# Kernel tuning notes

Measured on AMD Instinct MI355X. Metric: run time of the kernel, lower is better.

The kernel has to match this reference:

```python
import jax, jax.numpy as jnp
import numpy as np

B, S, C, H = 2, 2048, 1024, 16
D = C // H  # head_size = 64


def setup_inputs() -> dict:
    key = jax.random.key(0)
    ks = jax.random.split(key, 8)
    scale = 1.0 / np.sqrt(C)
    return {
        "src": jax.random.normal(ks[0], (B, S, C), dtype=jnp.float32),
        "Wq": jax.random.normal(ks[1], (C, C), dtype=jnp.float32) * scale,
        "bq": jnp.zeros((C,), dtype=jnp.float32),
        "Wk": jax.random.normal(ks[2], (C, C), dtype=jnp.float32) * scale,
        "bk": jnp.zeros((C,), dtype=jnp.float32),
        "Wv": jax.random.normal(ks[3], (C, C), dtype=jnp.float32) * scale,
        "bv": jnp.zeros((C,), dtype=jnp.float32),
        "rel_k_table": jax.random.normal(ks[4], (2 * S - 1, D), dtype=jnp.float32),
    }


def reference(src, Wq, bq, Wk, bk, Wv, bv, rel_k_table):
    # Linear projections (torch Linear: x @ W.T + b)
    q = src @ Wq.T + bq  # (B,S,C)
    k = src @ Wk.T + bk
    v = src @ Wv.T + bv
    # Faithful to torch .view: raw reshape (B,S,C) -> (B,H,S,D), NOT a transpose split
    q = q.reshape(B, H, S, D)
    k = k.reshape(B, H, S, D)
    v = v.reshape(B, H, S, D)
    # content score: q @ k^T
    content = jnp.einsum("bhsd,bhtd->bhst", q, k)  # (B,H,S,S)
    # relative-position embeddings: (S,S,D)
    pos = jnp.arange(S)
    shifted = pos[None, :] - pos[:, None] + (S - 1)  # (S,S) in [0, 2S-2]
    rel_k = rel_k_table[shifted]  # (S,S,D)
    # q.view(S, B*H, D) @ rel_k.permute(0,2,1): batched over first (query-pos) axis
    q_r = q.reshape(S, B * H, D)
    pos_score = jnp.einsum("sbd,std->sbt", q_r, rel_k)  # (S,BH,S)
    pos_score = jnp.transpose(pos_score, (1, 0, 2)).reshape(B, H, S, S)
    scores = (content + pos_score) / jnp.sqrt(jnp.float32(D))
    attn = jax.nn.softmax(scores, axis=-1)
    out = jnp.einsum("bhst,bhtd->bhsd", attn, v)  # (B,H,S,D)
    out = jnp.transpose(out, (0, 2, 1, 3)).reshape(B, S, C)
    return out
```

## Files before the change

### kernel.cpp

```cpp
#include <hip/hip_runtime.h>
#include <hip/hip_bf16.h>

#define BATCH 2
#define SEQ   2048
#define CH    1024
#define NH    16
#define HD    64
#define BHN   (BATCH*NH)
#define SD    (SEQ*HD)

typedef short v8s __attribute__((ext_vector_type(8)));
typedef short v4s __attribute__((ext_vector_type(4)));
typedef float v4f __attribute__((ext_vector_type(4)));

__device__ __forceinline__ short f2bf(float f) {
    unsigned u = __float_as_uint(f);
    u += 0x7fff + ((u >> 16) & 1);
    return (short)(u >> 16);
}

__device__ __forceinline__ unsigned pk2bf(float a, float b) {
    __hip_bfloat162 h = __float22bfloat162_rn(make_float2(a, b));
    unsigned u;
    __builtin_memcpy(&u, &h, 4);
    return u;
}

__device__ __forceinline__ float ex2(float x) {
    float r; asm("v_exp_f32 %0, %1" : "=v"(r) : "v"(x)); return r;
}

#if __has_builtin(__builtin_amdgcn_perm)
#define PERMB(a, b, s) __builtin_amdgcn_perm((a), (b), (s))
#else
__device__ __forceinline__ unsigned PERMB(unsigned a, unsigned b, unsigned s) {
    unsigned r = 0;
#pragma unroll
    for (int i = 0; i < 4; i++) {
        unsigned sb = (s >> (8 * i)) & 0xff, byte;
        if (sb >= 12) byte = (sb == 12) ? 0u : 0xffu;
        else if (sb < 4) byte = (b >> (8 * sb)) & 0xff;
        else byte = (a >> (8 * (sb - 4))) & 0xff;
        r |= byte << (8 * i);
    }
    return r;
}
#endif

__device__ __forceinline__ void gl_lds16(const short* g, short* l) {
    __builtin_amdgcn_global_load_lds(
        (const __attribute__((address_space(1))) void*)g,
        (__attribute__((address_space(3))) void*)l, 16, 0, 0);
}

__global__ __launch_bounds__(256) void cast_all_kernel(
    const float* __restrict__ src, const float* __restrict__ wq,
    const float* __restrict__ wk, const float* __restrict__ wv,
    const float* __restrict__ rel,
    short* __restrict__ xb, short* __restrict__ wqb,
    short* __restrict__ wkb, short* __restrict__ wvb,
    short* __restrict__ relb)
{
    const int z = blockIdx.z;
    const float* s; short* d; int n4;
    switch (z) {
        case 0: s = src; d = xb;   n4 = 1048576; break;
        case 1: s = wq;  d = wqb;  n4 = 262144;  break;
        case 2: s = wk;  d = wkb;  n4 = 262144;  break;
        case 3: s = wv;  d = wvb;  n4 = 262144;  break;
        default: s = rel; d = relb; n4 = 65520;  break;
    }
    for (int i = blockIdx.x * 256 + threadIdx.x; i < n4; i += gridDim.x * 256) {
        float4 v = ((const float4*)s)[i];
        v4s o; o.x = f2bf(v.x); o.y = f2bf(v.y); o.z = f2bf(v.z); o.w = f2bf(v.w);
        ((v4s*)d)[i] = o;
    }
}

__global__ __launch_bounds__(256, 3) void proj_mfma_kernel(
    const short* __restrict__ Xb,
    const short* __restrict__ Wqb, const short* __restrict__ Wkb,
    const short* __restrict__ Wvb,
    const float* __restrict__ bq, const float* __restrict__ bk,
    const float* __restrict__ bv,
    short* __restrict__ qo, short* __restrict__ ko, short* __restrict__ vo)
{
    const int z = blockIdx.z;
    const short* W    = (z == 0) ? Wqb : (z == 1) ? Wkb : Wvb;
    const float* bias = (z == 0) ? bq  : (z == 1) ? bk  : bv;
    short*       out  = (z == 0) ? qo  : (z == 1) ? ko  : vo;
    const float  osc  = (z == 0) ? 0.125f * 1.44269504088896f : 1.0f;

    const int m0 = blockIdx.x * 128;
    const int n0 = blockIdx.y * 128;
    const int tid  = threadIdx.x;
    const int w    = tid >> 6;
    const int lane = tid & 63;
    const int l15  = lane & 15;
    const int quad = lane >> 4;
    const int wm = w & 1, wn = w >> 1;

    __shared__ short Al[128 * 32];
    __shared__ short Bl[128 * 32];

    v4f acc[4][4];
#pragma unroll
    for (int i = 0; i < 4; i++)
#pragma unroll
        for (int j = 0; j < 4; j++) acc[i][j] = (v4f)(0.f);

    const int lr = lane >> 2;
    const int lc = (lane & 3) * 8;

    for (int k0 = 0; k0 < 1024; k0 += 32) {
        __syncthreads();
#pragma unroll
        for (int l = 0; l < 2; l++) {
            const int slab = w * 32 + l * 16;
            gl_lds16(Xb + (size_t)(m0 + slab + lr) * 1024 + k0 + lc,
                     &Al[slab * 32]);
            gl_lds16(W + (size_t)(n0 + slab + lr) * 1024 + k0 + lc,
                     &Bl[slab * 32]);
        }
        __syncthreads();
        v8s af[4], bf[4];
#pragma unroll
        for (int mt = 0; mt < 4; mt++)
            af[mt] = *(const v8s*)&Al[(wm * 64 + mt * 16 + l15) * 32 + quad * 8];
#pragma unroll
        for (int nt = 0; nt < 4; nt++)
            bf[nt] = *(const v8s*)&Bl[(wn * 64 + nt * 16 + l15) * 32 + quad * 8];
#pragma unroll
        for (int mt = 0; mt < 4; mt++)
#pragma unroll
            for (int nt = 0; nt < 4; nt++)
                acc[mt][nt] = __builtin_amdgcn_mfma_f32_16x16x32_bf16(
                    af[mt], bf[nt], acc[mt][nt], 0, 0, 0);
    }

    float bv4[4];
#pragma unroll
    for (int nt = 0; nt < 4; nt++)
        bv4[nt] = bias[n0 + wn * 64 + nt * 16 + l15];
#pragma unroll
    for (int mt = 0; mt < 4; mt++)
#pragma unroll
        for (int rg = 0; rg < 4; rg++) {
            const int row = m0 + wm * 64 + mt * 16 + quad * 4 + rg;
#pragma unroll
            for (int nt = 0; nt < 4; nt++)
                out[(size_t)row * 1024 + n0 + wn * 64 + nt * 16 + l15] =
                    f2bf((acc[mt][nt][rg] + bv4[nt]) * osc);
        }
}

__global__ __launch_bounds__(256) void vtrans_kernel(
    const short* __restrict__ v, short* __restrict__ vt)
{
    const int bh = blockIdx.y;
    const int t0 = blockIdx.x * 64;
    const int r = threadIdx.x >> 3;
    const int c = (threadIdx.x & 7) * 8;

    __shared__ short T[64][72];
    *(v8s*)&T[r][c] =
        *(const v8s*)(v + (size_t)bh * SD + (size_t)(t0 + r) * HD + c);
    *(v8s*)&T[r + 32][c] =
        *(const v8s*)(v + (size_t)bh * SD + (size_t)(t0 + r + 32) * HD + c);
    __syncthreads();
    v8s o0, o1;
#pragma unroll
    for (int e = 0; e < 8; e++) {
        const int t = 2 * (threadIdx.x & 7) + (e >> 2) + 16 * (e & 3);
        o0[e] = T[t][r];
        o1[e] = T[t][r + 32];
    }
    *(v8s*)(vt + (size_t)bh * SD + (size_t)r * SEQ + t0 + c) = o0;
    *(v8s*)(vt + (size_t)bh * SD + (size_t)(r + 32) * SEQ + t0 + c) = o1;
}

__global__ __launch_bounds__(256, 2) void attn_mfma_kernel(
    const short* __restrict__ qb, const short* __restrict__ kb,
    const short* __restrict__ vtb, const short* __restrict__ relb,
    float* __restrict__ out)
{
    const int tid  = threadIdx.x;
    const int w    = tid >> 6;
    const int lane = tid & 63;
    const int l15  = lane & 15;
    const int quad = lane >> 4;
    const int bh = blockIdx.x, b = bh >> 4, h = bh & 15;
    const int s0 = blockIdx.y * 128;
    const int i0 = w * 32;

    __shared__ short Kl[2][64][64];
    __shared__ short Vl[2][64][64];
    __shared__ short Rl[256][64];
    __shared__ short Pb[4][2][16][64];

    v8s qc_f[2][2], qr_f[2][2];
#pragma unroll
    for (int mt = 0; mt < 2; mt++)
#pragma unroll
    for (int kh = 0; kh < 2; kh++) {
        const int row = s0 + i0 + mt * 16 + l15;
        qc_f[mt][kh] = *(const v8s*)(qb + (size_t)bh * SD +
                                     (size_t)row * HD + kh * 32 + quad * 8);
        qr_f[mt][kh] = *(const v8s*)(qb + (size_t)row * (BHN * HD) +
                                     bh * HD + kh * 32 + quad * 8);
    }

    int      slv4[4];
    unsigned selA[4], selB[4], pwoff[4];
#pragma unroll
    for (int rg = 0; rg < 4; rg++) {
        const int ii = quad * 4 + rg;
        const int e  = l15 + 15 - ii;
        const bool lo = (e < 16);
        slv4[rg] = (quad * 16 + (e & 15)) << 2;
        selA[rg] = lo ? 0x05040c0cu : 0x07060c0cu;
        selB[rg] = lo ? 0x07060c0cu : 0x01000c0cu;
        pwoff[rg] = (unsigned)(w * 4096 + ii * 128 +
                    ((((l15 >> 1) ^ (ii & 7)) << 4) + ((l15 & 1) << 3)));
    }

    const int swz = (quad ^ (l15 & 7)) << 4;
    int kaddr[2][4];
#pragma unroll
    for (int kh = 0; kh < 2; kh++) {
        const int x = kh << 6;
#pragma unroll
        for (int nt = 0; nt < 4; nt++)
            kaddr[kh][nt] = (((nt * 16 + l15) << 7) + swz) ^ x;
    }
    const int paddr0 = (l15 << 7) + swz;

    const int Bq = 1920 - s0;
    int raddr[6];
#pragma unroll
    for (int st = 0; st < 6; st++) {
        const int lg = 2032 - s0 - i0 - 16 + st * 16 + l15;
        raddr[st] = ((lg & 255) << 7) + ((quad ^ (lg & 7)) << 4);
    }

    const int strow = tid >> 3;
    const int stc   = ((tid & 7) ^ (strow & 7)) * 8;
    const short* ksrc = kb  + (size_t)bh * SD + (size_t)strow * HD  + stc;
    const short* vsrc = vtb + (size_t)bh * SD + (size_t)strow * SEQ + stc;

#pragma unroll
    for (int g = 0; g < 3; g++) {
        const int r0 = Bq + g * 64 + strow;
        const int ra = r0 < 4094 ? r0 : 4094;
        const int rb2 = (r0 + 32) < 4094 ? (r0 + 32) : 4094;
        const unsigned sl = (unsigned)((Bq + g * 64 + w * 8) & 255) << 7;
        gl_lds16(relb + (size_t)ra * HD + stc, (short*)((char*)Rl + sl));
        gl_lds16(relb + (size_t)rb2 * HD + stc, (short*)((char*)Rl + sl + 4096));
    }
    gl_lds16(ksrc,              &Kl[0][w * 8][0]);
    gl_lds16(ksrc + 32 * HD,    &Kl[0][32 + w * 8][0]);
    gl_lds16(vsrc,              &Vl[0][w * 8][0]);
    gl_lds16(vsrc + 32 * SEQ,   &Vl[0][32 + w * 8][0]);

    const short* kp = ksrc + 4096;
    const short* vp = vsrc + 64;
    const char*  relbp = (const char*)relb + stc * 2;
    unsigned roff = (unsigned)(Bq + 192 + strow) * 128;
    const unsigned ROMAX = 4094u * 128;
    unsigned rlds = (unsigned)((Bq + 192 + w * 8) & 255) << 7;

    v4f o_acc[2][4];
#pragma unroll
    for (int mt = 0; mt < 2; mt++)
#pragma unroll
        for (int nt = 0; nt < 4; nt++) o_acc[mt][nt] = (v4f)(0.f);
    float lpart[2][4] = {{0.f,0.f,0.f,0.f},{0.f,0.f,0.f,0.f}};

    v4f cacc[2][4], racc[2][5];
    unsigned g01[2][4], g23[2][4], g4v[2][4];

    auto ZACC = [&]() {
#pragma unroll
        for (int mt = 0; mt < 2; mt++) {
#pragma unroll
            for (int nt = 0; nt < 4; nt++) cacc[mt][nt] = (v4f)(0.f);
#pragma unroll
            for (int jt = 0; jt < 5; jt++) racc[mt][jt] = (v4f)(0.f);
        }
    };

    auto STAGE_K = [&](int dst) {
        short* kd = &Kl[0][w * 8][0] + (dst << 12);
        gl_lds16(kp,            kd);
        gl_lds16(kp + 32 * HD,  kd + 32 * 64);
        unsigned rc0 = roff < ROMAX ? roff : ROMAX;
        unsigned rc1 = (roff + 4096) < ROMAX ? (roff + 4096) : ROMAX;
        gl_lds16((const short*)(relbp + rc0), (short*)((char*)Rl + rlds));
        gl_lds16((const short*)(relbp + rc1), (short*)((char*)Rl + rlds + 4096));
        kp += 4096; roff += 8192; rlds = (rlds + 8192) & 32767;
    };

    auto STAGE_V = [&](int dst) {
        short* vd = &Vl[0][w * 8][0] + (dst << 12);
        gl_lds16(vp,            vd);
        gl_lds16(vp + 32 * SEQ, vd + 32 * 64);
        vp += 64;
    };

    auto QK = [&](int cur) {
        const char* kbase = (const char*)Kl + cur * 8192;
        const char* rbase = (const char*)Rl;
#pragma unroll
        for (int kh = 0; kh < 2; kh++) {
            v8s kf[4], rfj[6];
#pragma unroll
            for (int nt = 0; nt < 4; nt++)
                kf[nt] = *(const v8s*)(kbase + kaddr[kh][nt]);
#pragma unroll
            for (int st = 0; st < 6; st++)
                rfj[st] = *(const v8s*)(rbase + (raddr[st] ^ (kh << 6)));
            __builtin_amdgcn_s_setprio(1);
#pragma unroll
            for (int mt = 0; mt < 2; mt++)
#pragma unroll
                for (int nt = 0; nt < 4; nt++)
                    cacc[mt][nt] = __builtin_amdgcn_mfma_f32_16x16x32_bf16(
                        qc_f[mt][kh], kf[nt], cacc[mt][nt], 0, 0, 0);
#pragma unroll
            for (int jt = 0; jt < 5; jt++)
                racc[0][jt] = __builtin_amdgcn_mfma_f32_16x16x32_bf16(
                    qr_f[0][kh], rfj[jt + 1], racc[0][jt], 0, 0, 0);
#pragma unroll
            for (int jt = 0; jt < 5; jt++)
                racc[1][jt] = __builtin_amdgcn_mfma_f32_16x16x32_bf16(
                    qr_f[1][kh], rfj[jt], racc[1][jt], 0, 0, 0);
            __builtin_amdgcn_s_setprio(0);
        }
#pragma unroll
        for (int st = 0; st < 6; st++) raddr[st] = (raddr[st] + 8192) & 32767;
    };

    auto PHASE1 = [&]() {
#pragma unroll
        for (int mt = 0; mt < 2; mt++)
#pragma unroll
        for (int rg = 0; rg < 4; rg++) {
            unsigned p01 = pk2bf(racc[mt][0][rg], racc[mt][1][rg]);
            unsigned p23 = pk2bf(racc[mt][2][rg], racc[mt][3][rg]);
            unsigned p4  = pk2bf(racc[mt][4][rg], racc[mt][4][rg]);
            g01[mt][rg] = (unsigned)__builtin_amdgcn_ds_bpermute(slv4[rg], (int)p01);
            g23[mt][rg] = (unsigned)__builtin_amdgcn_ds_bpermute(slv4[rg], (int)p23);
            g4v[mt][rg] = (unsigned)__builtin_amdgcn_ds_bpermute(slv4[rg], (int)p4);
        }
    };

    auto PHASE2 = [&]() {
#pragma unroll
        for (int mt = 0; mt < 2; mt++)
#pragma unroll
        for (int rg = 0; rg < 4; rg++) {
            const unsigned a01 = g01[mt][rg], a23 = g23[mt][rg], a4 = g4v[mt][rg];
            unsigned pb0 = PERMB(a01, a01, selA[rg]);
            unsigned pb1 = PERMB(a01, a23, selB[rg]);
            unsigned pb2 = PERMB(a23, a23, selA[rg]);
            unsigned pb3 = PERMB(a23, a4,  selB[rg]);
            float p0 = ex2(cacc[mt][0][rg] + __uint_as_float(pb0));
            float p1 = ex2(cacc[mt][1][rg] + __uint_as_float(pb1));
            float p2 = ex2(cacc[mt][2][rg] + __uint_as_float(pb2));
            float p3 = ex2(cacc[mt][3][rg] + __uint_as_float(pb3));
            lpart[mt][rg] += (p0 + p1) + (p2 + p3);
            *(uint2*)((char*)Pb + pwoff[rg] + mt * 2048) =
                make_uint2(pk2bf(p0, p1), pk2bf(p2, p3));
        }
    };

    auto PV = [&](int vbuf) {
        const char* vbase = (const char*)Vl + vbuf * 8192;
        const char* pbW = (const char*)Pb + w * 4096;
#pragma unroll
        for (int kh = 0; kh < 2; kh++) {
            v8s vf[4];
#pragma unroll
            for (int nt = 0; nt < 4; nt++)
                vf[nt] = *(const v8s*)(vbase + kaddr[kh][nt]);
            v8s pa0 = *(const v8s*)(pbW + (paddr0 ^ (kh << 6)));
            v8s pa1 = *(const v8s*)(pbW + 2048 + (paddr0 ^ (kh << 6)));
            __builtin_amdgcn_s_setprio(1);
#pragma unroll
            for (int nt = 0; nt < 4; nt++)
                o_acc[0][nt] = __builtin_amdgcn_mfma_f32_16x16x32_bf16(
                    pa0, vf[nt], o_acc[0][nt], 0, 0, 0);
#pragma unroll
            for (int nt = 0; nt < 4; nt++)
                o_acc[1][nt] = __builtin_amdgcn_mfma_f32_16x16x32_bf16(
                    pa1, vf[nt], o_acc[1][nt], 0, 0, 0);
            __builtin_amdgcn_s_setprio(0);
        }
    };

    __syncthreads();
    STAGE_K(1);
    STAGE_V(1);
    ZACC(); QK(0); PHASE1(); PHASE2();

    int cur = 0;
    for (int t0 = 64; t0 < SEQ; t0 += 64) {
        cur ^= 1;
        __syncthreads();
        STAGE_K(cur ^ 1);
        ZACC(); QK(cur);
        PHASE1();
        PV(cur ^ 1);
        __syncthreads();
        STAGE_V(cur ^ 1);
        PHASE2();
    }
    PV(cur);

#pragma unroll
    for (int mt = 0; mt < 2; mt++)
#pragma unroll
    for (int rg = 0; rg < 4; rg++) {
        float rs = lpart[mt][rg];
#pragma unroll
        for (int off = 1; off < 16; off <<= 1)
            rs += __shfl_xor(rs, off);
        const float inv = 1.f / rs;
        const int row = s0 + i0 + mt * 16 + quad * 4 + rg;
        const size_t base = ((size_t)b * SEQ + row) * CH + h * HD;
#pragma unroll
        for (int nt = 0; nt < 4; nt++)
            out[base + nt * 16 + l15] = o_acc[mt][nt][rg] * inv;
    }
}

extern "C" void kernel_launch(void* const* d_in, const int* in_sizes, int n_in,
                              void* d_out, int out_size, void* d_ws, size_t ws_size,
                              hipStream_t stream)
{
    const float* src  = (const float*)d_in[0];
    const float* Wq   = (const float*)d_in[1];
    const float* bq   = (const float*)d_in[2];
    const float* Wk   = (const float*)d_in[3];
    const float* bk   = (const float*)d_in[4];
    const float* Wv   = (const float*)d_in[5];
    const float* bv   = (const float*)d_in[6];
    const float* relk = (const float*)d_in[7];
    float* out = (float*)d_out;

    const size_t nQKV = (size_t)BATCH * SEQ * CH;
    const size_t nW   = (size_t)CH * CH;
    short* qb   = (short*)d_ws;
    short* kb   = qb + nQKV;
    short* vb   = kb + nQKV;
    short* vtb  = vb + nQKV;
    short* xb   = vtb + nQKV;
    short* wqb  = xb + nQKV;
    short* wkb  = wqb + nW;
    short* wvb  = wkb + nW;
    short* relb = wvb + nW;

    cast_all_kernel<<<dim3(512, 1, 5), 256, 0, stream>>>(
        src, Wq, Wk, Wv, relk, xb, wqb, wkb, wvb, relb);

    dim3 gProj(4096 / 128, 1024 / 128, 3);
    proj_mfma_kernel<<<gProj, 256, 0, stream>>>(
        xb, wqb, wkb, wvb, bq, bk, bv, qb, kb, vb);

    dim3 gVt(SEQ / 64, BHN);
    vtrans_kernel<<<gVt, 256, 0, stream>>>(vb, vtb);

    dim3 gAttn(BHN, SEQ / 128);
    attn_mfma_kernel<<<gAttn, 256, 0, stream>>>(qb, kb, vtb, relb, out);
}
```

Measured before the change: 208.7 us.

## Load K, V and rel-pos fragments directly from global into registers, drop LDS staging

Removes the shared-memory double-buffered staging of K, V and the relative-position table and their block barriers. Each wave now loads its MFMA operand fragments straight from global memory into registers, one tile ahead, with sched_barrier fences around the loads to keep them interleaved with compute. This removes the LDS round-trips and the __syncthreads, but every wave now fetches K/V/rel tiles independently, which multiplies global/L2 traffic by the number of waves. It also raises register pressure because of the prefetched fragment arrays. The last iteration issues prefetches past the end of K and V.

```diff
diff --git a/kernel.cpp b/kernel.cpp
--- a/kernel.cpp
+++ b/kernel.cpp
@@ -12,6 +12,8 @@
 typedef short v8s __attribute__((ext_vector_type(8)));
 typedef short v4s __attribute__((ext_vector_type(4)));
 typedef float v4f __attribute__((ext_vector_type(4)));
+
+#define SCHED0() __builtin_amdgcn_sched_barrier(0)
 
 __device__ __forceinline__ short f2bf(float f) {
     unsigned u = __float_as_uint(f);
@@ -193,9 +195,6 @@
     const int s0 = blockIdx.y * 128;
     const int i0 = w * 32;
 
-    __shared__ short Kl[2][64][64];
-    __shared__ short Vl[2][64][64];
-    __shared__ short Rl[256][64];
     __shared__ short Pb[4][2][16][64];
 
     v8s qc_f[2][2], qr_f[2][2];
@@ -223,51 +222,48 @@
         pwoff[rg] = (unsigned)(w * 4096 + ii * 128 +
                     ((((l15 >> 1) ^ (ii & 7)) << 4) + ((l15 & 1) << 3)));
     }
-
-    const int swz = (quad ^ (l15 & 7)) << 4;
-    int kaddr[2][4];
-#pragma unroll
-    for (int kh = 0; kh < 2; kh++) {
-        const int x = kh << 6;
-#pragma unroll
-        for (int nt = 0; nt < 4; nt++)
-            kaddr[kh][nt] = (((nt * 16 + l15) << 7) + swz) ^ x;
-    }
-    const int paddr0 = (l15 << 7) + swz;
-
-    const int Bq = 1920 - s0;
-    int raddr[6];
-#pragma unroll
-    for (int st = 0; st < 6; st++) {
-        const int lg = 2032 - s0 - i0 - 16 + st * 16 + l15;
-        raddr[st] = ((lg & 255) << 7) + ((quad ^ (lg & 7)) << 4);
-    }
-
-    const int strow = tid >> 3;
-    const int stc   = ((tid & 7) ^ (strow & 7)) * 8;
-    const short* ksrc = kb  + (size_t)bh * SD + (size_t)strow * HD  + stc;
-    const short* vsrc = vtb + (size_t)bh * SD + (size_t)strow * SEQ + stc;
-
-#pragma unroll
-    for (int g = 0; g < 3; g++) {
-        const int r0 = Bq + g * 64 + strow;
-        const int ra = r0 < 4094 ? r0 : 4094;
-        const int rb2 = (r0 + 32) < 4094 ? (r0 + 32) : 4094;
-        const unsigned sl = (unsigned)((Bq + g * 64 + w * 8) & 255) << 7;
-        gl_lds16(relb + (size_t)ra * HD + stc, (short*)((char*)Rl + sl));
-        gl_lds16(relb + (size_t)rb2 * HD + stc, (short*)((char*)Rl + sl + 4096));
-    }
-    gl_lds16(ksrc,              &Kl[0][w * 8][0]);
-    gl_lds16(ksrc + 32 * HD,    &Kl[0][32 + w * 8][0]);
-    gl_lds16(vsrc,              &Vl[0][w * 8][0]);
-    gl_lds16(vsrc + 32 * SEQ,   &Vl[0][32 + w * 8][0]);
-
-    const short* kp = ksrc + 4096;
-    const short* vp = vsrc + 64;
-    const char*  relbp = (const char*)relb + stc * 2;
-    unsigned roff = (unsigned)(Bq + 192 + strow) * 128;
-    const unsigned ROMAX = 4094u * 128;
-    unsigned rlds = (unsigned)((Bq + 192 + w * 8) & 255) << 7;
+    const int paddr0 = (l15 << 7) + ((quad ^ (l15 & 7)) << 4);
+
+    unsigned koff = (unsigned)bh * SD + (unsigned)l15 * HD + quad * 8;
+    unsigned voff[4];
+#pragma unroll
+    for (int nt = 0; nt < 4; nt++)
+        voff[nt] = (unsigned)bh * SD + (unsigned)(nt * 16 + l15) * SEQ + quad * 8;
+    unsigned roffs[6];
+#pragma unroll
+    for (int st = 0; st < 6; st++)
+        roffs[st] = (unsigned)(2032 - s0 - i0 - 16 + st * 16 + l15) * HD + quad * 8;
+    const unsigned RMAX = 4094u * HD;
+
+    v8s kfp[2][4], vfp[2][4], rfp[6][2];
+
+    auto LOAD_K = [&]() {
+#pragma unroll
+        for (int kh = 0; kh < 2; kh++)
+#pragma unroll
+            for (int nt = 0; nt < 4; nt++)
+                kfp[kh][nt] = *(const v8s*)(kb + koff + nt * 1024 + kh * 32);
+        koff += 4096;
+    };
+    auto LOAD_V = [&]() {
+#pragma unroll
+        for (int kh = 0; kh < 2; kh++)
+#pragma unroll
+            for (int nt = 0; nt < 4; nt++)
+                vfp[kh][nt] = *(const v8s*)(vtb + voff[nt] + kh * 32);
+#pragma unroll
+        for (int nt = 0; nt < 4; nt++) voff[nt] += 64;
+    };
+    auto LOAD_R = [&]() {
+#pragma unroll
+        for (int st = 0; st < 6; st++) {
+            const unsigned c = roffs[st] < RMAX ? roffs[st] : RMAX;
+#pragma unroll
+            for (int kh = 0; kh < 2; kh++)
+                rfp[st][kh] = *(const v8s*)(relb + c + kh * 32);
+            roffs[st] += 4096;
+        }
+    };
 
     v4f o_acc[2][4];
 #pragma unroll
@@ -276,68 +272,42 @@
         for (int nt = 0; nt < 4; nt++) o_acc[mt][nt] = (v4f)(0.f);
     float lpart[2][4] = {{0.f,0.f,0.f,0.f},{0.f,0.f,0.f,0.f}};
 
+    const v4f vz = (v4f)(0.f);
+
     v4f cacc[2][4], racc[2][5];
     unsigned g01[2][4], g23[2][4], g4v[2][4];
 
-    auto ZACC = [&]() {
-#pragma unroll
-        for (int mt = 0; mt < 2; mt++) {
-#pragma unroll
-            for (int nt = 0; nt < 4; nt++) cacc[mt][nt] = (v4f)(0.f);
-#pragma unroll
-            for (int jt = 0; jt < 5; jt++) racc[mt][jt] = (v4f)(0.f);
-        }
-    };
-
-    auto STAGE_K = [&](int dst) {
-        short* kd = &Kl[0][w * 8][0] + (dst << 12);
-        gl_lds16(kp,            kd);
-        gl_lds16(kp + 32 * HD,  kd + 32 * 64);
-        unsigned rc0 = roff < ROMAX ? roff : ROMAX;
-        unsigned rc1 = (roff + 4096) < ROMAX ? (roff + 4096) : ROMAX;
-        gl_lds16((const short*)(relbp + rc0), (short*)((char*)Rl + rlds));
-        gl_lds16((const short*)(relbp + rc1), (short*)((char*)Rl + rlds + 4096));
-        kp += 4096; roff += 8192; rlds = (rlds + 8192) & 32767;
-    };
-
-    auto STAGE_V = [&](int dst) {
-        short* vd = &Vl[0][w * 8][0] + (dst << 12);
-        gl_lds16(vp,            vd);
-        gl_lds16(vp + 32 * SEQ, vd + 32 * 64);
-        vp += 64;
-    };
-
-    auto QK = [&](int cur) {
-        const char* kbase = (const char*)Kl + cur * 8192;
-        const char* rbase = (const char*)Rl;
-#pragma unroll
-        for (int kh = 0; kh < 2; kh++) {
-            v8s kf[4], rfj[6];
-#pragma unroll
-            for (int nt = 0; nt < 4; nt++)
-                kf[nt] = *(const v8s*)(kbase + kaddr[kh][nt]);
-#pragma unroll
-            for (int st = 0; st < 6; st++)
-                rfj[st] = *(const v8s*)(rbase + (raddr[st] ^ (kh << 6)));
-            __builtin_amdgcn_s_setprio(1);
-#pragma unroll
-            for (int mt = 0; mt < 2; mt++)
-#pragma unroll
-                for (int nt = 0; nt < 4; nt++)
-                    cacc[mt][nt] = __builtin_amdgcn_mfma_f32_16x16x32_bf16(
-                        qc_f[mt][kh], kf[nt], cacc[mt][nt], 0, 0, 0);
-#pragma unroll
-            for (int jt = 0; jt < 5; jt++)
-                racc[0][jt] = __builtin_amdgcn_mfma_f32_16x16x32_bf16(
-                    qr_f[0][kh], rfj[jt + 1], racc[0][jt], 0, 0, 0);
-#pragma unroll
-            for (int jt = 0; jt < 5; jt++)
-                racc[1][jt] = __builtin_amdgcn_mfma_f32_16x16x32_bf16(
-                    qr_f[1][kh], rfj[jt], racc[1][jt], 0, 0, 0);
-            __builtin_amdgcn_s_setprio(0);
-        }
-#pragma unroll
-        for (int st = 0; st < 6; st++) raddr[st] = (raddr[st] + 8192) & 32767;
+    auto QK = [&]() {
+        __builtin_amdgcn_s_setprio(1);
+#pragma unroll
+        for (int mt = 0; mt < 2; mt++)
+#pragma unroll
+            for (int nt = 0; nt < 4; nt++)
+                cacc[mt][nt] = __builtin_amdgcn_mfma_f32_16x16x32_bf16(
+                    qc_f[mt][0], kfp[0][nt], vz, 0, 0, 0);
+#pragma unroll
+        for (int jt = 0; jt < 5; jt++)
+            racc[0][jt] = __builtin_amdgcn_mfma_f32_16x16x32_bf16(
+                qr_f[0][0], rfp[jt + 1][0], vz, 0, 0, 0);
+#pragma unroll
+        for (int jt = 0; jt < 5; jt++)
+            racc[1][jt] = __builtin_amdgcn_mfma_f32_16x16x32_bf16(
+                qr_f[1][0], rfp[jt][0], vz, 0, 0, 0);
+#pragma unroll
+        for (int mt = 0; mt < 2; mt++)
+#pragma unroll
+            for (int nt = 0; nt < 4; nt++)
+                cacc[mt][nt] = __builtin_amdgcn_mfma_f32_16x16x32_bf16(
+                    qc_f[mt][1], kfp[1][nt], cacc[mt][nt], 0, 0, 0);
+#pragma unroll
+        for (int jt = 0; jt < 5; jt++)
+            racc[0][jt] = __builtin_amdgcn_mfma_f32_16x16x32_bf16(
+                qr_f[0][1], rfp[jt + 1][1], racc[0][jt], 0, 0, 0);
+#pragma unroll
+        for (int jt = 0; jt < 5; jt++)
+            racc[1][jt] = __builtin_amdgcn_mfma_f32_16x16x32_bf16(
+                qr_f[1][1], rfp[jt][1], racc[1][jt], 0, 0, 0);
+        __builtin_amdgcn_s_setprio(0);
     };
 
     auto PHASE1 = [&]() {
@@ -374,48 +344,45 @@
         }
     };
 
-    auto PV = [&](int vbuf) {
-        const char* vbase = (const char*)Vl + vbuf * 8192;
+    auto PV = [&]() {
         const char* pbW = (const char*)Pb + w * 4096;
 #pragma unroll
         for (int kh = 0; kh < 2; kh++) {
-            v8s vf[4];
-#pragma unroll
-            for (int nt = 0; nt < 4; nt++)
-                vf[nt] = *(const v8s*)(vbase + kaddr[kh][nt]);
             v8s pa0 = *(const v8s*)(pbW + (paddr0 ^ (kh << 6)));
             v8s pa1 = *(const v8s*)(pbW + 2048 + (paddr0 ^ (kh << 6)));
             __builtin_amdgcn_s_setprio(1);
 #pragma unroll
             for (int nt = 0; nt < 4; nt++)
                 o_acc[0][nt] = __builtin_amdgcn_mfma_f32_16x16x32_bf16(
-                    pa0, vf[nt], o_acc[0][nt], 0, 0, 0);
+                    pa0, vfp[kh][nt], o_acc[0][nt], 0, 0, 0);
 #pragma unroll
             for (int nt = 0; nt < 4; nt++)
                 o_acc[1][nt] = __builtin_amdgcn_mfma_f32_16x16x32_bf16(
-                    pa1, vf[nt], o_acc[1][nt], 0, 0, 0);
+                    pa1, vfp[kh][nt], o_acc[1][nt], 0, 0, 0);
             __builtin_amdgcn_s_setprio(0);
         }
     };
 
-    __syncthreads();
-    STAGE_K(1);
-    STAGE_V(1);
-    ZACC(); QK(0); PHASE1(); PHASE2();
-
-    int cur = 0;
+    LOAD_K();
+    LOAD_R();
+    LOAD_V();
+
+    QK();
+    SCHED0(); LOAD_K(); SCHED0();
+    PHASE1();
+    SCHED0(); LOAD_R(); SCHED0();
+    PHASE2();
+
     for (int t0 = 64; t0 < SEQ; t0 += 64) {
-        cur ^= 1;
-        __syncthreads();
-        STAGE_K(cur ^ 1);
-        ZACC(); QK(cur);
+        QK();
+        SCHED0(); LOAD_K(); SCHED0();
         PHASE1();
-        PV(cur ^ 1);
-        __syncthreads();
-        STAGE_V(cur ^ 1);
+        SCHED0(); LOAD_R(); SCHED0();
+        PV();
+        SCHED0(); LOAD_V(); SCHED0();
         PHASE2();
     }
-    PV(cur);
+    PV();
 
 #pragma unroll
     for (int mt = 0; mt < 2; mt++)
```

Result: slower. 370.2 us (+77.4%).
